# Kernel optimization log

Measured on AMD Instinct MI355X. Metric: run time of the kernel, lower is better.

Reference implementation:

```python
import jax, jax.numpy as jnp
import numpy as np

DIM = 4096
BATCH = 64
DEFAULT_LR = 0.001
DEFAULT_ALPHA = 0.01
EPS = 1e-08


def setup_inputs() -> dict:
    key = jax.random.key(0)
    k1, k2, k3 = jax.random.split(key, 3)
    weight = jax.random.normal(k1, (DIM, DIM), dtype=jnp.float32)
    input_x = jax.random.normal(k2, (BATCH, DIM), dtype=jnp.float32)
    grad = jax.random.normal(k3, (DIM, DIM), dtype=jnp.float32)
    return {"weight": weight, "input_x": input_x, "grad": grad}


def reference(weight, input_x, grad):
    # L2-normalize inputs along last dim (normalize_inputs=True)
    x = input_x / (jnp.linalg.norm(input_x, axis=-1, keepdims=True) + EPS)
    # batched outer product averaged over batch: (dim, dim)
    outer = jnp.einsum('bi,bj->ij', x, x) / x.shape[0]
    decay_matrix = jnp.eye(DIM, dtype=weight.dtype) - DEFAULT_ALPHA * outer
    # W_{t+1} = W @ (I - alpha * outer) - lr * grad
    new_weight = weight @ decay_matrix - DEFAULT_LR * grad
    return new_weight
```

## Files before the change

kernel.cpp:

```cpp
#include <hip/hip_runtime.h>
#include <math.h>

#define DIM 4096
#define BATCH 64

typedef __attribute__((ext_vector_type(8))) short short8;
typedef __attribute__((ext_vector_type(4))) float f32x4;
typedef __attribute__((ext_vector_type(4))) unsigned int u32x4;

__device__ __forceinline__ float4 ld4(const float* p) {
    return *reinterpret_cast<const float4*>(p);
}

__device__ __forceinline__ unsigned short f2bf(float f) {
    unsigned u = __builtin_bit_cast(unsigned, f);
    u = (u + 0x7fffu + ((u >> 16) & 1u)) >> 16;
    return (unsigned short)u;
}

__device__ __forceinline__ unsigned pack_bf2(float x, float y) {
    return (__builtin_bit_cast(unsigned, x) >> 16) |
           (__builtin_bit_cast(unsigned, y) & 0xffff0000u);
}

__global__ __launch_bounds__(256) void k_norm(const float* __restrict__ x,
                                              unsigned short* __restrict__ xb1,
                                              unsigned short* __restrict__ xa2) {
    const int b = blockIdx.x;
    const int tid = threadIdx.x;
    const float* row = x + (size_t)b * DIM;

    float ss = 0.f;
    for (int k = tid * 4; k < DIM; k += 256 * 4) {
        float4 v = ld4(row + k);
        ss += v.x * v.x + v.y * v.y + v.z * v.z + v.w * v.w;
    }
#pragma unroll
    for (int m = 32; m >= 1; m >>= 1) ss += __shfl_xor(ss, m, 64);

    __shared__ float wsum[4];
    if ((tid & 63) == 0) wsum[tid >> 6] = ss;
    __syncthreads();
    const float total = wsum[0] + wsum[1] + wsum[2] + wsum[3];
    const float scale = 1.0f / (sqrtf(total) + 1e-8f);

    const int bt = b >> 4;
    const int li = b & 15;
    const int ks  = b >> 5;
    const int bhi = (b >> 3) & 3;
    const int br  = b & 7;

    for (int k = tid; k < DIM; k += 256) {
        const float v = row[k] * scale;
        const unsigned short h = f2bf(v);
        const int l1 = li | (((k & 31) >> 3) << 4);
        xb1[(size_t)((((bt * 128) + (k >> 5)) * 64 + l1) << 3) + (k & 7)] = h;
        const int l2 = (k & 15) | (bhi << 4);
        xa2[(size_t)(((((k >> 4) * 2) + ks) * 64 + l2) << 3) + br] = h;
    }
}

__global__ __launch_bounds__(1024, 4) void k_fused(const float* __restrict__ W,
                                                   const float* __restrict__ G,
                                                   const unsigned short* __restrict__ xb1,
                                                   const unsigned short* __restrict__ xa2,
                                                   float* __restrict__ out) {
    __shared__ __align__(16) float yp[16 * 4 * 64 * 4];
    __shared__ float y2[16 * 68];

    const int tid = threadIdx.x;
    const int wv = tid >> 6;
    const int l  = tid & 63;
    const int lr = l & 15;
    const int lh = l >> 4;
    const int i0 = blockIdx.x * 16;

    f32x4 acc0 = {0.f, 0.f, 0.f, 0.f};
    f32x4 acc1 = acc0, acc2 = acc0, acc3 = acc0;
    const short8* xb1v = (const short8*)xb1;

#pragma unroll 2
    for (int s = 0; s < 8; ++s) {
        const int kbg = wv * 8 + s;
        const float* wp = W + (size_t)(i0 + lr) * DIM + kbg * 32 + lh * 8;
        const float4 wa = ld4(wp);
        const float4 wb = ld4(wp + 4);
        const int bs = kbg * 64 + l;
        const short8 b0 = xb1v[bs];
        const short8 b1 = xb1v[bs + 8192];
        const short8 b2 = xb1v[bs + 16384];
        const short8 b3 = xb1v[bs + 24576];
        u32x4 ap;
        ap[0] = pack_bf2(wa.x, wa.y);
        ap[1] = pack_bf2(wa.z, wa.w);
        ap[2] = pack_bf2(wb.x, wb.y);
        ap[3] = pack_bf2(wb.z, wb.w);
        const short8 a = __builtin_bit_cast(short8, ap);
        acc0 = __builtin_amdgcn_mfma_f32_16x16x32_bf16(a, b0, acc0, 0, 0, 0);
        acc1 = __builtin_amdgcn_mfma_f32_16x16x32_bf16(a, b1, acc1, 0, 0, 0);
        acc2 = __builtin_amdgcn_mfma_f32_16x16x32_bf16(a, b2, acc2, 0, 0, 0);
        acc3 = __builtin_amdgcn_mfma_f32_16x16x32_bf16(a, b3, acc3, 0, 0, 0);
    }
    {
        f32x4* dst = (f32x4*)yp;
        dst[(wv * 4 + 0) * 64 + l] = acc0;
        dst[(wv * 4 + 1) * 64 + l] = acc1;
        dst[(wv * 4 + 2) * 64 + l] = acc2;
        dst[(wv * 4 + 3) * 64 + l] = acc3;
    }
    __syncthreads();

    {
        const int r  = tid >> 6;
        const int bb = tid & 63;
        const int btt = bb >> 4;
        const int lii = (bb & 15) | ((r >> 2) << 4);
        const int jq  = r & 3;
        float s = 0.f;
#pragma unroll
        for (int w = 0; w < 16; ++w) s += yp[(((w * 4 + btt) * 64 + lii) << 2) + jq];
        y2[r * 68 + bb] = s;
    }
    __syncthreads();

    const float NC = -0.01f / 64.0f;
    short8 ya0, ya1;
#pragma unroll
    for (int j = 0; j < 8; ++j) {
        ya0[j] = (short)f2bf(NC * y2[lr * 68 + lh * 8 + j]);
        ya1[j] = (short)f2bf(NC * y2[lr * 68 + 32 + lh * 8 + j]);
    }

    constexpr float LRc = 0.001f;
    const short8* xa2v = (const short8*)xa2;
#pragma unroll 4
    for (int t = 0; t < 16; ++t) {
        const int jt = wv * 16 + t;
        const short8 a0 = xa2v[(jt * 2 + 0) * 64 + l];
        const short8 a1 = xa2v[(jt * 2 + 1) * 64 + l];
        f32x4 d = {0.f, 0.f, 0.f, 0.f};
        d = __builtin_amdgcn_mfma_f32_16x16x32_bf16(a0, ya0, d, 0, 0, 0);
        d = __builtin_amdgcn_mfma_f32_16x16x32_bf16(a1, ya1, d, 0, 0, 0);
        const size_t idx = (size_t)(i0 + lr) * DIM + jt * 16 + lh * 4;
        const float4 w4 = ld4(W + idx);
        const float4 g4 = ld4(G + idx);
        float4 o;
        o.x = w4.x - LRc * g4.x + d[0];
        o.y = w4.y - LRc * g4.y + d[1];
        o.z = w4.z - LRc * g4.z + d[2];
        o.w = w4.w - LRc * g4.w + d[3];
        *reinterpret_cast<float4*>(out + idx) = o;
    }
}

extern "C" void kernel_launch(void* const* d_in, const int* in_sizes, int n_in,
                              void* d_out, int out_size, void* d_ws, size_t ws_size,
                              hipStream_t stream) {
    const float* W = (const float*)d_in[0];
    const float* X = (const float*)d_in[1];
    const float* G = (const float*)d_in[2];
    float* out = (float*)d_out;

    unsigned short* xb1 = (unsigned short*)d_ws;
    unsigned short* xa2 = xb1 + (size_t)DIM * BATCH;

    hipLaunchKernelGGL(k_norm, dim3(BATCH), dim3(256), 0, stream, X, xb1, xa2);
    hipLaunchKernelGGL(k_fused, dim3(DIM / 16), dim3(1024), 0, stream,
                       W, G, xb1, xa2, out);
}
```

Measured before the change: 61.61 us.

## Split fused kernel into split-K projection, fragment reduce, and update kernels

Replaces the single 1024-thread fused kernel with three kernels. One computes W·Xᵀ partials over four K-chunks with 256-thread blocks and hoisted W loads. A small kernel reduces the partials and packs the bf16 MFMA fragments, and an update kernel with a 256x4 grid batches the W and G loads before the MFMA and write. This raises the block count and memory-level parallelism at the cost of two extra launches, a global partial-sum buffer, and a second read of W.

```diff
diff --git a/kernel.cpp b/kernel.cpp
--- a/kernel.cpp
+++ b/kernel.cpp
@@ -60,96 +60,148 @@
     }
 }
 
-__global__ __launch_bounds__(1024, 4) void k_fused(const float* __restrict__ W,
-                                                   const float* __restrict__ G,
-                                                   const unsigned short* __restrict__ xb1,
-                                                   const unsigned short* __restrict__ xa2,
-                                                   float* __restrict__ out) {
-    __shared__ __align__(16) float yp[16 * 4 * 64 * 4];
-    __shared__ float y2[16 * 68];
+__global__ __launch_bounds__(256, 4) void k_wxt(const float* __restrict__ W,
+                                                const unsigned short* __restrict__ xb1,
+                                                float* __restrict__ ypart) {
+    __shared__ f32x4 yp[4][4][64];
 
     const int tid = threadIdx.x;
-    const int wv = tid >> 6;
-    const int l  = tid & 63;
+    const int w = tid >> 6;
+    const int l = tid & 63;
     const int lr = l & 15;
     const int lh = l >> 4;
-    const int i0 = blockIdx.x * 16;
+    const int rt = blockIdx.x;
+    const int kc = blockIdx.y;
+    const int i0 = rt * 16;
+
+    float4 wa[8], wb[8];
+    const float* wp0 = W + (size_t)(i0 + lr) * DIM + (kc * 32 + w * 8) * 32 + lh * 8;
+#pragma unroll
+    for (int s = 0; s < 8; ++s) {
+        wa[s] = ld4(wp0 + s * 32);
+        wb[s] = ld4(wp0 + s * 32 + 4);
+    }
 
     f32x4 acc0 = {0.f, 0.f, 0.f, 0.f};
     f32x4 acc1 = acc0, acc2 = acc0, acc3 = acc0;
     const short8* xb1v = (const short8*)xb1;
 
-#pragma unroll 2
+#pragma unroll
     for (int s = 0; s < 8; ++s) {
-        const int kbg = wv * 8 + s;
-        const float* wp = W + (size_t)(i0 + lr) * DIM + kbg * 32 + lh * 8;
-        const float4 wa = ld4(wp);
-        const float4 wb = ld4(wp + 4);
+        const int kbg = kc * 32 + w * 8 + s;
         const int bs = kbg * 64 + l;
         const short8 b0 = xb1v[bs];
         const short8 b1 = xb1v[bs + 8192];
         const short8 b2 = xb1v[bs + 16384];
         const short8 b3 = xb1v[bs + 24576];
         u32x4 ap;
-        ap[0] = pack_bf2(wa.x, wa.y);
-        ap[1] = pack_bf2(wa.z, wa.w);
-        ap[2] = pack_bf2(wb.x, wb.y);
-        ap[3] = pack_bf2(wb.z, wb.w);
+        ap[0] = pack_bf2(wa[s].x, wa[s].y);
+        ap[1] = pack_bf2(wa[s].z, wa[s].w);
+        ap[2] = pack_bf2(wb[s].x, wb[s].y);
+        ap[3] = pack_bf2(wb[s].z, wb[s].w);
         const short8 a = __builtin_bit_cast(short8, ap);
         acc0 = __builtin_amdgcn_mfma_f32_16x16x32_bf16(a, b0, acc0, 0, 0, 0);
         acc1 = __builtin_amdgcn_mfma_f32_16x16x32_bf16(a, b1, acc1, 0, 0, 0);
         acc2 = __builtin_amdgcn_mfma_f32_16x16x32_bf16(a, b2, acc2, 0, 0, 0);
         acc3 = __builtin_amdgcn_mfma_f32_16x16x32_bf16(a, b3, acc3, 0, 0, 0);
     }
+    yp[w][0][l] = acc0;
+    yp[w][1][l] = acc1;
+    yp[w][2][l] = acc2;
+    yp[w][3][l] = acc3;
+    __syncthreads();
+
     {
-        f32x4* dst = (f32x4*)yp;
-        dst[(wv * 4 + 0) * 64 + l] = acc0;
-        dst[(wv * 4 + 1) * 64 + l] = acc1;
-        dst[(wv * 4 + 2) * 64 + l] = acc2;
-        dst[(wv * 4 + 3) * 64 + l] = acc3;
-    }
-    __syncthreads();
-
-    {
-        const int r  = tid >> 6;
         const int bb = tid & 63;
         const int btt = bb >> 4;
-        const int lii = (bb & 15) | ((r >> 2) << 4);
-        const int jq  = r & 3;
-        float s = 0.f;
-#pragma unroll
-        for (int w = 0; w < 16; ++w) s += yp[(((w * 4 + btt) * 64 + lii) << 2) + jq];
-        y2[r * 68 + bb] = s;
-    }
-    __syncthreads();
-
+        const int rb = tid >> 6;
+#pragma unroll
+        for (int q = 0; q < 4; ++q) {
+            const int r = rb * 4 + q;
+            const int lii = (bb & 15) | ((r >> 2) << 4);
+            const int jq = r & 3;
+            float s = yp[0][btt][lii][jq] + yp[1][btt][lii][jq]
+                    + yp[2][btt][lii][jq] + yp[3][btt][lii][jq];
+            ypart[((size_t)kc * DIM + (i0 + r)) * 64 + bb] = s;
+        }
+    }
+}
+
+__global__ __launch_bounds__(256) void k_yfrag(const float* __restrict__ ypart,
+                                               unsigned short* __restrict__ yab) {
+    const int gid = blockIdx.x * 256 + threadIdx.x;
+    const int rt = gid >> 6;
+    const int l = gid & 63;
+    const int lr = l & 15;
+    const int lh = l >> 4;
     const float NC = -0.01f / 64.0f;
-    short8 ya0, ya1;
-#pragma unroll
-    for (int j = 0; j < 8; ++j) {
-        ya0[j] = (short)f2bf(NC * y2[lr * 68 + lh * 8 + j]);
-        ya1[j] = (short)f2bf(NC * y2[lr * 68 + 32 + lh * 8 + j]);
-    }
-
+    short8* yabv = (short8*)yab;
+
+#pragma unroll
+    for (int h = 0; h < 2; ++h) {
+        float s[8] = {};
+#pragma unroll
+        for (int kc = 0; kc < 4; ++kc) {
+            const float* p = ypart + ((size_t)kc * DIM + (rt * 16 + lr)) * 64 + h * 32 + lh * 8;
+            const float4 f0 = ld4(p);
+            const float4 f1 = ld4(p + 4);
+            s[0] += f0.x; s[1] += f0.y; s[2] += f0.z; s[3] += f0.w;
+            s[4] += f1.x; s[5] += f1.y; s[6] += f1.z; s[7] += f1.w;
+        }
+        short8 fr;
+#pragma unroll
+        for (int j = 0; j < 8; ++j) fr[j] = (short)f2bf(NC * s[j]);
+        yabv[(size_t)(rt * 64 + l) * 2 + h] = fr;
+    }
+}
+
+__global__ __launch_bounds__(256, 4) void k_update(const float* __restrict__ W,
+                                                   const float* __restrict__ G,
+                                                   const unsigned short* __restrict__ xa2,
+                                                   const unsigned short* __restrict__ yab,
+                                                   float* __restrict__ out) {
+    const int tid = threadIdx.x;
+    const int wv = tid >> 6;
+    const int l = tid & 63;
+    const int lr = l & 15;
+    const int lh = l >> 4;
+    const int rt = blockIdx.x;
+    const int cc = blockIdx.y;
+    const int i0 = rt * 16;
+
+    const short8* yabv = (const short8*)yab;
+    const short8* xa2v = (const short8*)xa2;
+    const short8 ya0 = yabv[(size_t)(rt * 64 + l) * 2];
+    const short8 ya1 = yabv[(size_t)(rt * 64 + l) * 2 + 1];
+
+    const size_t rowoff = (size_t)(i0 + lr) * DIM;
+    const int jt0 = cc * 64 + wv * 16;
     constexpr float LRc = 0.001f;
-    const short8* xa2v = (const short8*)xa2;
-#pragma unroll 4
-    for (int t = 0; t < 16; ++t) {
-        const int jt = wv * 16 + t;
-        const short8 a0 = xa2v[(jt * 2 + 0) * 64 + l];
-        const short8 a1 = xa2v[(jt * 2 + 1) * 64 + l];
-        f32x4 d = {0.f, 0.f, 0.f, 0.f};
-        d = __builtin_amdgcn_mfma_f32_16x16x32_bf16(a0, ya0, d, 0, 0, 0);
-        d = __builtin_amdgcn_mfma_f32_16x16x32_bf16(a1, ya1, d, 0, 0, 0);
-        const size_t idx = (size_t)(i0 + lr) * DIM + jt * 16 + lh * 4;
-        const float4 w4 = ld4(W + idx);
-        const float4 g4 = ld4(G + idx);
-        float4 o;
-        o.x = w4.x - LRc * g4.x + d[0];
-        o.y = w4.y - LRc * g4.y + d[1];
-        o.z = w4.z - LRc * g4.z + d[2];
-        o.w = w4.w - LRc * g4.w + d[3];
-        *reinterpret_cast<float4*>(out + idx) = o;
+
+    for (int t0 = 0; t0 < 16; t0 += 8) {
+        float4 w8[8], g8[8];
+#pragma unroll
+        for (int i = 0; i < 8; ++i) {
+            const size_t idx = rowoff + (jt0 + t0 + i) * 16 + lh * 4;
+            w8[i] = ld4(W + idx);
+            g8[i] = ld4(G + idx);
+        }
+#pragma unroll
+        for (int i = 0; i < 8; ++i) {
+            const int jt = jt0 + t0 + i;
+            const short8 a0 = xa2v[(size_t)(jt * 2 + 0) * 64 + l];
+            const short8 a1 = xa2v[(size_t)(jt * 2 + 1) * 64 + l];
+            f32x4 d = {0.f, 0.f, 0.f, 0.f};
+            d = __builtin_amdgcn_mfma_f32_16x16x32_bf16(a0, ya0, d, 0, 0, 0);
+            d = __builtin_amdgcn_mfma_f32_16x16x32_bf16(a1, ya1, d, 0, 0, 0);
+            const size_t idx = rowoff + jt * 16 + lh * 4;
+            float4 o;
+            o.x = w8[i].x - LRc * g8[i].x + d[0];
+            o.y = w8[i].y - LRc * g8[i].y + d[1];
+            o.z = w8[i].z - LRc * g8[i].z + d[2];
+            o.w = w8[i].w - LRc * g8[i].w + d[3];
+            *reinterpret_cast<float4*>(out + idx) = o;
+        }
     }
 }
 
@@ -163,8 +215,12 @@
 
     unsigned short* xb1 = (unsigned short*)d_ws;
     unsigned short* xa2 = xb1 + (size_t)DIM * BATCH;
+    unsigned short* yab = xa2 + (size_t)DIM * BATCH;
+    float* ypart = (float*)(yab + (size_t)DIM * BATCH);
 
     hipLaunchKernelGGL(k_norm, dim3(BATCH), dim3(256), 0, stream, X, xb1, xa2);
-    hipLaunchKernelGGL(k_fused, dim3(DIM / 16), dim3(1024), 0, stream,
-                       W, G, xb1, xa2, out);
-}
+    hipLaunchKernelGGL(k_wxt, dim3(256, 4), dim3(256), 0, stream, W, xb1, ypart);
+    hipLaunchKernelGGL(k_yfrag, dim3(64), dim3(256), 0, stream, ypart, yab);
+    hipLaunchKernelGGL(k_update, dim3(256, 4), dim3(256), 0, stream,
+                       W, G, xa2, yab, out);
+}
```

Result: slower. 83.20 us (+35.0%).

## Split row tiles across two blocks, swizzle block ids, stage epilogue through LDS

Applied to the files above, without the earlier changes.

Doubles the grid so each 16-row tile is handled by two blocks, each writing half of the columns. Block ids are swizzled so the two halves of a tile land on different XCD groups. The epilogue swaps MFMA operand order and stages the correction tile through LDS, so each lane then writes row-contiguous float4 chunks for coalesced W/G loads and output stores. The cost is that the first GEMM (W·X^T) is now computed twice per row tile, and the epilogue gains an extra barrier and LDS round-trip.

```diff
diff --git a/kernel.cpp b/kernel.cpp
--- a/kernel.cpp
+++ b/kernel.cpp
@@ -25,7 +25,7 @@
 
 __global__ __launch_bounds__(256) void k_norm(const float* __restrict__ x,
                                               unsigned short* __restrict__ xb1,
-                                              unsigned short* __restrict__ xa2) {
+                                              unsigned short* __restrict__ xb2) {
     const int b = blockIdx.x;
     const int tid = threadIdx.x;
     const float* row = x + (size_t)b * DIM;
@@ -46,34 +46,40 @@
 
     const int bt = b >> 4;
     const int li = b & 15;
-    const int ks  = b >> 5;
-    const int bhi = (b >> 3) & 3;
-    const int br  = b & 7;
+    const int ks = b >> 5;
+    const int hi = (b & 31) >> 3;
+    const int jr = b & 7;
 
     for (int k = tid; k < DIM; k += 256) {
         const float v = row[k] * scale;
         const unsigned short h = f2bf(v);
         const int l1 = li | (((k & 31) >> 3) << 4);
         xb1[(size_t)((((bt * 128) + (k >> 5)) * 64 + l1) << 3) + (k & 7)] = h;
-        const int l2 = (k & 15) | (bhi << 4);
-        xa2[(size_t)(((((k >> 4) * 2) + ks) * 64 + l2) << 3) + br] = h;
-    }
-}
-
-__global__ __launch_bounds__(1024, 4) void k_fused(const float* __restrict__ W,
+        const int l2 = (k & 15) | (hi << 4);
+        xb2[(size_t)(((((k >> 4) * 2) + ks) * 64 + l2) << 3) + jr] = h;
+    }
+}
+
+__global__ __launch_bounds__(1024, 8) void k_fused(const float* __restrict__ W,
                                                    const float* __restrict__ G,
                                                    const unsigned short* __restrict__ xb1,
-                                                   const unsigned short* __restrict__ xa2,
+                                                   const unsigned short* __restrict__ xb2,
                                                    float* __restrict__ out) {
-    __shared__ __align__(16) float yp[16 * 4 * 64 * 4];
-    __shared__ float y2[16 * 68];
+    __shared__ __align__(16) float lds[17472];
+    float* yp = lds;
+    float* y2 = lds + 16384;
 
     const int tid = threadIdx.x;
     const int wv = tid >> 6;
     const int l  = tid & 63;
     const int lr = l & 15;
     const int lh = l >> 4;
-    const int i0 = blockIdx.x * 16;
+
+    const int bid = blockIdx.x;
+    const int sid = (bid & 7) * 64 + (bid >> 3);
+    const int rt  = sid >> 1;
+    const int half = sid & 1;
+    const int i0 = rt * 16;
 
     f32x4 acc0 = {0.f, 0.f, 0.f, 0.f};
     f32x4 acc1 = acc0, acc2 = acc0, acc3 = acc0;
@@ -130,26 +136,51 @@
         ya0[j] = (short)f2bf(NC * y2[lr * 68 + lh * 8 + j]);
         ya1[j] = (short)f2bf(NC * y2[lr * 68 + 32 + lh * 8 + j]);
     }
+    __syncthreads();
 
     constexpr float LRc = 0.001f;
-    const short8* xa2v = (const short8*)xa2;
-#pragma unroll 4
-    for (int t = 0; t < 16; ++t) {
-        const int jt = wv * 16 + t;
-        const short8 a0 = xa2v[(jt * 2 + 0) * 64 + l];
-        const short8 a1 = xa2v[(jt * 2 + 1) * 64 + l];
-        f32x4 d = {0.f, 0.f, 0.f, 0.f};
-        d = __builtin_amdgcn_mfma_f32_16x16x32_bf16(a0, ya0, d, 0, 0, 0);
-        d = __builtin_amdgcn_mfma_f32_16x16x32_bf16(a1, ya1, d, 0, 0, 0);
-        const size_t idx = (size_t)(i0 + lr) * DIM + jt * 16 + lh * 4;
-        const float4 w4 = ld4(W + idx);
-        const float4 g4 = ld4(G + idx);
-        float4 o;
-        o.x = w4.x - LRc * g4.x + d[0];
-        o.y = w4.y - LRc * g4.y + d[1];
-        o.z = w4.z - LRc * g4.z + d[2];
-        o.w = w4.w - LRc * g4.w + d[3];
-        *reinterpret_cast<float4*>(out + idx) = o;
+    const short8* xb2v = (const short8*)xb2;
+    float* dl = lds + wv * 1088;
+    const int colbase = half * 2048 + wv * 128;
+    const int cc4 = (l & 15) * 4;
+    const int rr0 = l >> 4;
+
+    for (int c = 0; c < 2; ++c) {
+        const int col0 = colbase + c * 64;
+        const int jt0 = col0 >> 4;
+        f32x4 dt[4];
+#pragma unroll
+        for (int tl = 0; tl < 4; ++tl) {
+            const int bslot = (jt0 + tl) * 128 + l;
+            f32x4 d = {0.f, 0.f, 0.f, 0.f};
+            d = __builtin_amdgcn_mfma_f32_16x16x32_bf16(ya0, xb2v[bslot], d, 0, 0, 0);
+            d = __builtin_amdgcn_mfma_f32_16x16x32_bf16(ya1, xb2v[bslot + 64], d, 0, 0, 0);
+            dt[tl] = d;
+        }
+#pragma unroll
+        for (int tl = 0; tl < 4; ++tl)
+#pragma unroll
+            for (int q = 0; q < 4; ++q)
+                dl[(lh * 4 + q) * 68 + tl * 16 + lr] = dt[tl][q];
+
+        float4 w4[4], g4[4];
+#pragma unroll
+        for (int i = 0; i < 4; ++i) {
+            const size_t gidx = (size_t)(i0 + rr0 + 4 * i) * DIM + col0 + cc4;
+            w4[i] = ld4(W + gidx);
+            g4[i] = ld4(G + gidx);
+        }
+#pragma unroll
+        for (int i = 0; i < 4; ++i) {
+            const float4 dd = ld4(dl + (rr0 + 4 * i) * 68 + cc4);
+            const size_t gidx = (size_t)(i0 + rr0 + 4 * i) * DIM + col0 + cc4;
+            float4 o;
+            o.x = w4[i].x - LRc * g4[i].x + dd.x;
+            o.y = w4[i].y - LRc * g4[i].y + dd.y;
+            o.z = w4[i].z - LRc * g4[i].z + dd.z;
+            o.w = w4[i].w - LRc * g4[i].w + dd.w;
+            *reinterpret_cast<float4*>(out + gidx) = o;
+        }
     }
 }
 
@@ -162,9 +193,9 @@
     float* out = (float*)d_out;
 
     unsigned short* xb1 = (unsigned short*)d_ws;
-    unsigned short* xa2 = xb1 + (size_t)DIM * BATCH;
-
-    hipLaunchKernelGGL(k_norm, dim3(BATCH), dim3(256), 0, stream, X, xb1, xa2);
-    hipLaunchKernelGGL(k_fused, dim3(DIM / 16), dim3(1024), 0, stream,
-                       W, G, xb1, xa2, out);
-}
+    unsigned short* xb2 = xb1 + (size_t)DIM * BATCH;
+
+    hipLaunchKernelGGL(k_norm, dim3(BATCH), dim3(256), 0, stream, X, xb1, xb2);
+    hipLaunchKernelGGL(k_fused, dim3(512), dim3(1024), 0, stream,
+                       W, G, xb1, xb2, out);
+}
```

New measurement: 65.48 us. 1.06x slower.
